# Optimization experiments

Hardware: AMD Instinct MI355X
Metric: run time of the kernel (lower is better)

## Reference

```python
import jax, jax.numpy as jnp
import numpy as np

HEADS = 8
NUM_QUERY = 16

def setup_inputs() -> dict:
    key = jax.random.key(0)
    k1, k2, k3 = jax.random.split(key, 3)
    b, t, h, w, C = 8, 16, 32, 32, 256  # C = heads * c, c = 32
    q = NUM_QUERY
    btn_features = 256
    btn_enc = jax.random.normal(k1, (b, t, h, w, C), dtype=jnp.float32)
    btn_dec = jax.random.normal(k2, (b, q * t, C), dtype=jnp.float32)
    W = jax.random.normal(k3, (HEADS * q, btn_features), dtype=jnp.float32) * (1.0 / np.sqrt(HEADS * q))
    bias = jnp.zeros((btn_features,), dtype=jnp.float32)
    return {"btn_dec": btn_dec, "btn_enc": btn_enc, "W": W, "bias": bias}

def reference(btn_dec, btn_enc, W, bias):
    b, t, h, w, C = btn_enc.shape
    g = HEADS
    c = C // g
    q = btn_dec.shape[1] // t
    # b t h w (g c) -> b g t h w c
    enc = btn_enc.reshape(b, t, h, w, g, c).transpose(0, 4, 1, 2, 3, 5)
    # b (q t) (g c) -> b g q t c
    dec = btn_dec.reshape(b, q, t, g, c).transpose(0, 3, 1, 2, 4)
    # broadcast-mul + sum over c == batched contraction; output ordered (..., q, g)
    scores = jnp.einsum('bgqtc,bgthwc->bthwqg', dec, enc)  # [b,t,h,w,q,g]
    scores = scores.reshape(b, t * h * w, q * g)
    out = jax.nn.relu(scores @ W + bias)  # [b, t*h*w, btn_features]
    return out.reshape(b, t, h, w, -1)
```

## Files before the change

### kernel.cpp

```cpp
#include <hip/hip_runtime.h>


#define CCH 256
#define FF  256
#define HW  1024

typedef __bf16 bf16x8 __attribute__((ext_vector_type(8)));
typedef float  f32x4  __attribute__((ext_vector_type(4)));
typedef float  f32x16 __attribute__((ext_vector_type(16)));
typedef unsigned short u16x4 __attribute__((ext_vector_type(4)));
typedef unsigned short u16x8 __attribute__((ext_vector_type(8)));

__device__ __forceinline__ unsigned short f2bf(float f) {
    __bf16 b = (__bf16)f;
    return __builtin_bit_cast(unsigned short, b);
}

__global__ __launch_bounds__(256, 4) void attnmap_fused(
        const float* __restrict__ dec, const float* __restrict__ E,
        const float* __restrict__ W,  const float* __restrict__ bias,
        float* __restrict__ O) {
    const int id0 = blockIdx.x;
    const int id  = ((id0 & 7) << 7) | (id0 >> 3);
    const int bt = id >> 3;
    const int fq = (id >> 1) & 3;
    const int rh = id & 1;
    const int tid = threadIdx.x;
    const int lane = tid & 63, wq = tid >> 6;
    const int lr5 = lane & 31, kgr = lane >> 5;

    __shared__ unsigned short Bs[64 * 256];
    __shared__ unsigned short Et[4][32 * 32];

    {
        float* dstg = (float*)&Et[0][0];
        const float* decb = dec + (size_t)(bt >> 4) * 65536 + (size_t)(bt & 15) * 256;
        const int fl = tid & 63, sc = tid >> 6;
        for (int g = 0; g < 8; ++g) {
            if (tid < 128) {
                const int q = tid >> 3, seg = tid & 7;
                *reinterpret_cast<f32x4*>(&dstg[q * 32 + seg * 4]) =
                    *reinterpret_cast<const f32x4*>(decb + q * 4096 + g * 32 + seg * 4);
            }
            __syncthreads();
            float s[8];
            #pragma unroll
            for (int e = 0; e < 8; ++e) s[e] = 0.f;
            #pragma unroll
            for (int q = 0; q < 16; ++q) {
                const float w = W[(q * 8 + g) * FF + fq * 64 + fl];
                #pragma unroll
                for (int e = 0; e < 8; ++e) s[e] += dstg[q * 32 + sc * 8 + e] * w;
            }
            u16x8 m8;
            #pragma unroll
            for (int e = 0; e < 8; ++e) m8[e] = f2bf(s[e]);
            *reinterpret_cast<u16x8*>(&Bs[fl * 256 + ((g * 4 + sc) ^ (fl & 7)) * 8]) = m8;
            __syncthreads();
        }
    }

    const float* Ebt = E + (size_t)bt * (HW * CCH);
    float*       Obt = O + (size_t)bt * (HW * FF);
    const int rowbase = rh * 512 + wq * 128;
    unsigned short* Etw = &Et[wq][0];

    const float bv0 = bias[fq * 64 + lr5];
    const float bv1 = bias[fq * 64 + 32 + lr5];

    const int g_r8 = lane >> 3;
    const int g_s3 = lane & 7;
    const int bswz = lr5 & 7;
    const int eswz = lr5 & 3;
    const unsigned short* Bs0 = &Bs[lr5 * 256];
    const unsigned short* Bs1 = &Bs[(32 + lr5) * 256];
    const unsigned short* Etr = &Etw[lr5 * 32];

    f32x4 Sva[4], Svb[4];
    f32x16 acc0, acc1;

    auto GLOAD = [&](int it, f32x4 (&S)[4]) {
        const float* base = Ebt + (size_t)(rowbase + (it >> 3) * 32) * CCH
                          + (it & 7) * 32 + g_s3 * 4;
        #pragma unroll
        for (int i = 0; i < 4; ++i)
            S[i] = *reinterpret_cast<const f32x4*>(base + (size_t)(i * 8 + g_r8) * CCH);
    };
    auto EWRITE = [&](const f32x4 (&S)[4]) {
        #pragma unroll
        for (int i = 0; i < 4; ++i) {
            const int r = i * 8 + g_r8;
            u16x4 h = { f2bf(S[i][0]), f2bf(S[i][1]), f2bf(S[i][2]), f2bf(S[i][3]) };
            *reinterpret_cast<u16x4*>(
                &Etw[r * 32 + (((g_s3 >> 1) ^ (r & 3)) * 8) + (g_s3 & 1) * 4]) = h;
        }
    };
    auto COMPUTE = [&](int it) {
        const int kc = it & 7;
        if (kc == 0) { acc0 = (f32x16)0.f; acc1 = (f32x16)0.f; }
        #pragma unroll
        for (int kk = 0; kk < 2; ++kk) {
            const bf16x8 af = *reinterpret_cast<const bf16x8*>(
                &Etr[((kk * 2 + kgr) ^ eswz) * 8]);
            const bf16x8 b0 = *reinterpret_cast<const bf16x8*>(
                &Bs0[((kc * 4 + kk * 2 + kgr) ^ bswz) * 8]);
            const bf16x8 b1 = *reinterpret_cast<const bf16x8*>(
                &Bs1[((kc * 4 + kk * 2 + kgr) ^ bswz) * 8]);
            acc0 = __builtin_amdgcn_mfma_f32_32x32x16_bf16(af, b0, acc0, 0, 0, 0);
            acc1 = __builtin_amdgcn_mfma_f32_32x32x16_bf16(af, b1, acc1, 0, 0, 0);
        }
        if (kc == 7) {
            const int row0 = rowbase + (it >> 3) * 32 + 4 * kgr;
            #pragma unroll
            for (int reg = 0; reg < 16; ++reg) {
                const int r = row0 + (reg & 3) + 8 * (reg >> 2);
                float* op = Obt + (size_t)r * FF + fq * 64 + lr5;
                __builtin_nontemporal_store(fmaxf(acc0[reg] + bv0, 0.f), op);
                __builtin_nontemporal_store(fmaxf(acc1[reg] + bv1, 0.f), op + 32);
            }
        }
    };

    GLOAD(0, Sva);
    GLOAD(1, Svb);
    EWRITE(Sva);
    for (int itp = 0; itp < 32; itp += 2) {
        COMPUTE(itp);
        if (itp + 2 < 32) GLOAD(itp + 2, Sva);
        EWRITE(Svb);
        COMPUTE(itp + 1);
        if (itp + 3 < 32) GLOAD(itp + 3, Svb);
        if (itp + 2 < 32) EWRITE(Sva);
    }
}

extern "C" void kernel_launch(void* const* d_in, const int* in_sizes, int n_in,
                              void* d_out, int out_size, void* d_ws, size_t ws_size,
                              hipStream_t stream) {
    const float* dec  = (const float*)d_in[0];
    const float* enc  = (const float*)d_in[1];
    const float* W    = (const float*)d_in[2];
    const float* bias = (const float*)d_in[3];
    float* out = (float*)d_out;

    attnmap_fused<<<dim3(1024), dim3(256), 0, stream>>>(dec, enc, W, bias, out);
}
```

Baseline: 59.49 us.

## Deepen encoder prefetch to four register stages with double-buffered LDS tiles

Moves the per-wave encoder tile staging from two register buffers to four, so global loads are issued three iterations ahead. The LDS tile gains a second slot with an 8-way XOR swizzle, which lets a write target one slot while compute reads the other. Occupancy is lowered from 4 to 3 blocks per SM to make room for the extra registers. The aim is to hide global load latency in this bandwidth-bound kernel, at the cost of fewer resident waves.

```diff
diff --git a/kernel.cpp b/kernel.cpp
--- a/kernel.cpp
+++ b/kernel.cpp
@@ -16,7 +16,7 @@
     return __builtin_bit_cast(unsigned short, b);
 }
 
-__global__ __launch_bounds__(256, 4) void attnmap_fused(
+__global__ __launch_bounds__(256, 3) void attnmap_fused(
         const float* __restrict__ dec, const float* __restrict__ E,
         const float* __restrict__ W,  const float* __restrict__ bias,
         float* __restrict__ O) {
@@ -30,7 +30,7 @@
     const int lr5 = lane & 31, kgr = lane >> 5;
 
     __shared__ unsigned short Bs[64 * 256];
-    __shared__ unsigned short Et[4][32 * 32];
+    __shared__ unsigned short Et[4][32 * 64];
 
     {
         float* dstg = (float*)&Et[0][0];
@@ -71,12 +71,11 @@
     const int g_r8 = lane >> 3;
     const int g_s3 = lane & 7;
     const int bswz = lr5 & 7;
-    const int eswz = lr5 & 3;
+    const int eswz = lr5 & 7;
     const unsigned short* Bs0 = &Bs[lr5 * 256];
     const unsigned short* Bs1 = &Bs[(32 + lr5) * 256];
-    const unsigned short* Etr = &Etw[lr5 * 32];
+    const unsigned short* Etr = &Etw[lr5 * 64];
 
-    f32x4 Sva[4], Svb[4];
     f32x16 acc0, acc1;
 
     auto GLOAD = [&](int it, f32x4 (&S)[4]) {
@@ -86,22 +85,23 @@
         for (int i = 0; i < 4; ++i)
             S[i] = *reinterpret_cast<const f32x4*>(base + (size_t)(i * 8 + g_r8) * CCH);
     };
-    auto EWRITE = [&](const f32x4 (&S)[4]) {
+    auto EWRITE = [&](int it, const f32x4 (&S)[4]) {
+        const int p = it & 1;
         #pragma unroll
         for (int i = 0; i < 4; ++i) {
             const int r = i * 8 + g_r8;
             u16x4 h = { f2bf(S[i][0]), f2bf(S[i][1]), f2bf(S[i][2]), f2bf(S[i][3]) };
-            *reinterpret_cast<u16x4*>(
-                &Etw[r * 32 + (((g_s3 >> 1) ^ (r & 3)) * 8) + (g_s3 & 1) * 4]) = h;
+            const int slot = (p * 4 + (g_s3 >> 1)) ^ (r & 7);
+            *reinterpret_cast<u16x4*>(&Etw[r * 64 + slot * 8 + (g_s3 & 1) * 4]) = h;
         }
     };
     auto COMPUTE = [&](int it) {
-        const int kc = it & 7;
+        const int p = it & 1, kc = it & 7;
         if (kc == 0) { acc0 = (f32x16)0.f; acc1 = (f32x16)0.f; }
         #pragma unroll
         for (int kk = 0; kk < 2; ++kk) {
             const bf16x8 af = *reinterpret_cast<const bf16x8*>(
-                &Etr[((kk * 2 + kgr) ^ eswz) * 8]);
+                &Etr[((p * 4 + kk * 2 + kgr) ^ eswz) * 8]);
             const bf16x8 b0 = *reinterpret_cast<const bf16x8*>(
                 &Bs0[((kc * 4 + kk * 2 + kgr) ^ bswz) * 8]);
             const bf16x8 b1 = *reinterpret_cast<const bf16x8*>(
@@ -121,16 +121,22 @@
         }
     };
 
-    GLOAD(0, Sva);
-    GLOAD(1, Svb);
-    EWRITE(Sva);
-    for (int itp = 0; itp < 32; itp += 2) {
-        COMPUTE(itp);
-        if (itp + 2 < 32) GLOAD(itp + 2, Sva);
-        EWRITE(Svb);
-        COMPUTE(itp + 1);
-        if (itp + 3 < 32) GLOAD(itp + 3, Svb);
-        if (itp + 2 < 32) EWRITE(Sva);
+    f32x4 SA[4], SB[4], SC[4], SD[4];
+    GLOAD(0, SA); GLOAD(1, SB); GLOAD(2, SC); GLOAD(3, SD);
+    EWRITE(0, SA); EWRITE(1, SB);
+    for (int it4 = 0; it4 < 32; it4 += 4) {
+        COMPUTE(it4 + 0);
+        if (it4 + 4 < 32) GLOAD(it4 + 4, SA);
+        EWRITE(it4 + 2, SC);
+        COMPUTE(it4 + 1);
+        if (it4 + 5 < 32) GLOAD(it4 + 5, SB);
+        EWRITE(it4 + 3, SD);
+        COMPUTE(it4 + 2);
+        if (it4 + 6 < 32) GLOAD(it4 + 6, SC);
+        if (it4 + 4 < 32) EWRITE(it4 + 4, SA);
+        COMPUTE(it4 + 3);
+        if (it4 + 7 < 32) GLOAD(it4 + 7, SD);
+        if (it4 + 5 < 32) EWRITE(it4 + 5, SB);
     }
 }
 
```

Result: slower. 62.72 us (+5.4%).

## Split weight-combination precompute into separate kernel and load it via global_load_lds

Applied to the files above, without the earlier changes.

The per-(b,t) combined matrix M = dec·W is now computed once by a separate kernel into workspace in bf16, instead of being recomputed in every block. The GEMM kernel then copies its 64x256 slice straight into LDS with global_load_lds, and the grid grows to 4096 blocks of 128 rows each. This removes redundant FMA work and the many syncthreads from the prologue and adds parallelism. In exchange it pays for a second kernel launch, a workspace round trip, and a shorter main loop per block, so the Bs fill is amortised over fewer rows.

```diff
diff --git a/kernel.cpp b/kernel.cpp
--- a/kernel.cpp
+++ b/kernel.cpp
@@ -16,54 +16,79 @@
     return __builtin_bit_cast(unsigned short, b);
 }
 
-__global__ __launch_bounds__(256, 4) void attnmap_fused(
-        const float* __restrict__ dec, const float* __restrict__ E,
-        const float* __restrict__ W,  const float* __restrict__ bias,
-        float* __restrict__ O) {
+__device__ __forceinline__ void gload_lds16(const unsigned short* g, unsigned short* l) {
+    __builtin_amdgcn_global_load_lds(
+        (const __attribute__((address_space(1))) unsigned int*)g,
+        (__attribute__((address_space(3))) unsigned int*)l, 16, 0, 0);
+}
+
+__global__ __launch_bounds__(256) void compute_Mt_kernel(
+        const float* __restrict__ dec, const float* __restrict__ W,
+        unsigned short* __restrict__ Mt) {
+    const int j  = blockIdx.x;
+    const int bt = blockIdx.y;
+    const int b  = bt >> 4, t = bt & 15;
+    const int f  = threadIdx.x;
+    __shared__ float ldec[16][64];
+
+    const float* decbt = dec + (size_t)b * 65536 + (size_t)t * 256 + j * 64;
+    {
+        const int q = threadIdx.x >> 4, seg = threadIdx.x & 15;
+        const float4 v = *reinterpret_cast<const float4*>(decbt + q * 4096 + seg * 4);
+        *reinterpret_cast<float4*>(&ldec[q][seg * 4]) = v;
+    }
+    __syncthreads();
+
+    u16x8 rv[8];
+    #pragma unroll
+    for (int gi = 0; gi < 2; ++gi) {
+        const int g = j * 2 + gi;
+        float wv[16];
+        #pragma unroll
+        for (int q = 0; q < 16; ++q) wv[q] = W[(q * 8 + g) * FF + f];
+        #pragma unroll
+        for (int cc = 0; cc < 32; ++cc) {
+            float s = 0.f;
+            #pragma unroll
+            for (int q = 0; q < 16; ++q) s += ldec[q][gi * 32 + cc] * wv[q];
+            const int idx = gi * 32 + cc;
+            rv[idx >> 3][idx & 7] = f2bf(s);
+        }
+    }
+    unsigned short* dst = Mt + (size_t)bt * (FF * CCH) + (size_t)f * CCH + j * 64;
+    #pragma unroll
+    for (int s = 0; s < 8; ++s)
+        *reinterpret_cast<u16x8*>(dst + s * 8) = rv[s];
+}
+
+__global__ __launch_bounds__(256, 4) void gemm_tile_kernel(
+        const float* __restrict__ E, const unsigned short* __restrict__ Mt,
+        const float* __restrict__ bias, float* __restrict__ O) {
     const int id0 = blockIdx.x;
-    const int id  = ((id0 & 7) << 7) | (id0 >> 3);
-    const int bt = id >> 3;
-    const int fq = (id >> 1) & 3;
-    const int rh = id & 1;
+    const int id  = ((id0 & 7) << 9) | (id0 >> 3);
+    const int bt = id >> 5;
+    const int fq = (id >> 3) & 3;
+    const int rg = id & 7;
     const int tid = threadIdx.x;
     const int lane = tid & 63, wq = tid >> 6;
     const int lr5 = lane & 31, kgr = lane >> 5;
 
-    __shared__ unsigned short Bs[64 * 256];
-    __shared__ unsigned short Et[4][32 * 32];
+    const float*          Ebt = E  + (size_t)bt * (HW * CCH);
+    const unsigned short* Mtb = Mt + (size_t)bt * (FF * CCH) + (size_t)(fq * 64) * CCH;
+    float*                Obt = O  + (size_t)bt * (HW * FF);
 
-    {
-        float* dstg = (float*)&Et[0][0];
-        const float* decb = dec + (size_t)(bt >> 4) * 65536 + (size_t)(bt & 15) * 256;
-        const int fl = tid & 63, sc = tid >> 6;
-        for (int g = 0; g < 8; ++g) {
-            if (tid < 128) {
-                const int q = tid >> 3, seg = tid & 7;
-                *reinterpret_cast<f32x4*>(&dstg[q * 32 + seg * 4]) =
-                    *reinterpret_cast<const f32x4*>(decb + q * 4096 + g * 32 + seg * 4);
-            }
-            __syncthreads();
-            float s[8];
-            #pragma unroll
-            for (int e = 0; e < 8; ++e) s[e] = 0.f;
-            #pragma unroll
-            for (int q = 0; q < 16; ++q) {
-                const float w = W[(q * 8 + g) * FF + fq * 64 + fl];
-                #pragma unroll
-                for (int e = 0; e < 8; ++e) s[e] += dstg[q * 32 + sc * 8 + e] * w;
-            }
-            u16x8 m8;
-            #pragma unroll
-            for (int e = 0; e < 8; ++e) m8[e] = f2bf(s[e]);
-            *reinterpret_cast<u16x8*>(&Bs[fl * 256 + ((g * 4 + sc) ^ (fl & 7)) * 8]) = m8;
-            __syncthreads();
-        }
+    __shared__ __align__(16) unsigned short Bs[64 * 256];
+    __shared__ __align__(16) unsigned short Et[4][32 * 32];
+
+    #pragma unroll
+    for (int p = 0; p < 8; ++p) {
+        const int g = p * 256 + tid;
+        const int r = g >> 5, s = g & 31;
+        gload_lds16(Mtb + (size_t)r * CCH + ((s ^ (r & 7)) * 8), &Bs[g * 8]);
     }
+    __syncthreads();
 
-    const float* Ebt = E + (size_t)bt * (HW * CCH);
-    float*       Obt = O + (size_t)bt * (HW * FF);
-    const int rowbase = rh * 512 + wq * 128;
-    unsigned short* Etw = &Et[wq][0];
+    const int rowbase = rg * 128 + wq * 32;
 
     const float bv0 = bias[fq * 64 + lr5];
     const float bv1 = bias[fq * 64 + 32 + lr5];
@@ -74,14 +99,14 @@
     const int eswz = lr5 & 3;
     const unsigned short* Bs0 = &Bs[lr5 * 256];
     const unsigned short* Bs1 = &Bs[(32 + lr5) * 256];
+    unsigned short* Etw = &Et[wq][0];
     const unsigned short* Etr = &Etw[lr5 * 32];
 
     f32x4 Sva[4], Svb[4];
     f32x16 acc0, acc1;
 
     auto GLOAD = [&](int it, f32x4 (&S)[4]) {
-        const float* base = Ebt + (size_t)(rowbase + (it >> 3) * 32) * CCH
-                          + (it & 7) * 32 + g_s3 * 4;
+        const float* base = Ebt + (size_t)rowbase * CCH + (it & 7) * 32 + g_s3 * 4;
         #pragma unroll
         for (int i = 0; i < 4; ++i)
             S[i] = *reinterpret_cast<const f32x4*>(base + (size_t)(i * 8 + g_r8) * CCH);
@@ -110,7 +135,7 @@
             acc1 = __builtin_amdgcn_mfma_f32_32x32x16_bf16(af, b1, acc1, 0, 0, 0);
         }
         if (kc == 7) {
-            const int row0 = rowbase + (it >> 3) * 32 + 4 * kgr;
+            const int row0 = rowbase + 4 * kgr;
             #pragma unroll
             for (int reg = 0; reg < 16; ++reg) {
                 const int r = row0 + (reg & 3) + 8 * (reg >> 2);
@@ -124,13 +149,13 @@
     GLOAD(0, Sva);
     GLOAD(1, Svb);
     EWRITE(Sva);
-    for (int itp = 0; itp < 32; itp += 2) {
+    for (int itp = 0; itp < 8; itp += 2) {
         COMPUTE(itp);
-        if (itp + 2 < 32) GLOAD(itp + 2, Sva);
+        if (itp + 2 < 8) GLOAD(itp + 2, Sva);
         EWRITE(Svb);
         COMPUTE(itp + 1);
-        if (itp + 3 < 32) GLOAD(itp + 3, Svb);
-        if (itp + 2 < 32) EWRITE(Sva);
+        if (itp + 3 < 8) GLOAD(itp + 3, Svb);
+        if (itp + 2 < 8) EWRITE(Sva);
     }
 }
 
@@ -142,6 +167,8 @@
     const float* W    = (const float*)d_in[2];
     const float* bias = (const float*)d_in[3];
     float* out = (float*)d_out;
+    unsigned short* Mt = (unsigned short*)d_ws;
 
-    attnmap_fused<<<dim3(1024), dim3(256), 0, stream>>>(dec, enc, W, bias, out);
+    compute_Mt_kernel<<<dim3(4, 128), dim3(256), 0, stream>>>(dec, W, Mt);
+    gemm_tile_kernel<<<dim3(4096), dim3(256), 0, stream>>>(enc, Mt, bias, out);
 }
```

After: 61.21 us. +2.9%, slower.
